# Optimization experiments

Measured on AMD Instinct MI355X. Metric: run time of the kernel, lower is better.

## Reference

```python
import jax, jax.numpy as jnp
import numpy as np
import math

B, T, C = 2, 2048, 1024
H = 16
D = C // H  # 64


def setup_inputs() -> dict:
    key = jax.random.key(0)
    k1, k2, k3 = jax.random.split(key, 3)
    x = jax.random.normal(k1, (B, T, C), dtype=jnp.float32)
    W_attn = jax.random.normal(k2, (3 * C, C), dtype=jnp.float32) * (1.0 / math.sqrt(C))
    W_proj = jax.random.normal(k3, (C, C), dtype=jnp.float32) * (1.0 / math.sqrt(C))
    return {"x": x, "W_attn": W_attn, "W_proj": W_proj}


def reference(x, W_attn, W_proj):
    b, t, c = x.shape
    qkv = x @ W_attn.T                       # [B,T,3C]
    q, k, v = jnp.split(qkv, 3, axis=2)
    # [B,H,T,D]
    q = q.reshape(b, t, H, D).transpose(0, 2, 1, 3)
    k = k.reshape(b, t, H, D).transpose(0, 2, 1, 3)
    v = v.reshape(b, t, H, D).transpose(0, 2, 1, 3)
    scale = 1.0 / math.sqrt(D)
    P = jnp.einsum('bhqd,bhkd->bhqk', q, k) * scale   # [B,H,T,T]
    S = jax.nn.sigmoid(P)
    causal = jnp.tril(jnp.ones((t, t), dtype=bool))   # [T,T]
    S_lower = jnp.where(causal, S, 0.0)
    # suffix (reverse) cumulative sum along key axis
    Z = jax.lax.cumsum(S_lower, axis=3, reverse=True)
    P_prime = P - Z
    P_masked = jnp.where(causal, P_prime, -jnp.inf)
    att = jax.nn.softmax(P_masked, axis=-1)
    y = jnp.einsum('bhqk,bhkd->bhqd', att, v)         # [B,H,T,D]
    y = y.transpose(0, 2, 1, 3).reshape(b, t, c)
    return y @ W_proj.T
```

## Files before the change

### kernel.cpp

```cpp
#include <hip/hip_runtime.h>


typedef _Float16 h8 __attribute__((ext_vector_type(8)));
typedef _Float16 h4 __attribute__((ext_vector_type(4)));
typedef float f4 __attribute__((ext_vector_type(4)));

template <int CTRL>
__device__ __forceinline__ float dpp_shr_self(float x) {
  int xi = __builtin_bit_cast(int, x);
  return __builtin_bit_cast(float,
      __builtin_amdgcn_update_dpp(xi, xi, CTRL, 0xF, 0xF, false));
}
__device__ __forceinline__ float scan16_max(float x) {
  x = fmaxf(x, dpp_shr_self<0x111>(x));
  x = fmaxf(x, dpp_shr_self<0x112>(x));
  x = fmaxf(x, dpp_shr_self<0x114>(x));
  x = fmaxf(x, dpp_shr_self<0x118>(x));
  return x;
}
__device__ __forceinline__ float bcast15(float x) {
  return __builtin_bit_cast(float,
      __builtin_amdgcn_ds_swizzle(__builtin_bit_cast(int, x), 0x01F0));
}

__device__ __forceinline__ void gload_lds16(const _Float16* src, _Float16* dst_lds) {
  __builtin_amdgcn_global_load_lds(
      (const __attribute__((address_space(1))) void*)src,
      (__attribute__((address_space(3))) void*)dst_lds, 16, 0, 0);
}

__device__ __forceinline__ void vmcnt0_fence() {
  asm volatile("s_waitcnt vmcnt(0)" ::: "memory");
  __builtin_amdgcn_sched_barrier(0);
}

__global__ __launch_bounds__(256) void convert_all_kernel(const float* __restrict__ x,
                                                          const float* __restrict__ Wa,
                                                          const float* __restrict__ Wp,
                                                          _Float16* __restrict__ xh,
                                                          _Float16* __restrict__ wah,
                                                          _Float16* __restrict__ wph) {
  int i = blockIdx.x * 256 + threadIdx.x;
  const float* src;
  _Float16* dst;
  int off;
  if (i < 1048576) { src = x; dst = xh; off = i; }
  else if (i < 1048576 + 786432) { src = Wa; dst = wah; off = i - 1048576; }
  else { src = Wp; dst = wph; off = i - (1048576 + 786432); }
  f4 v = *(const f4*)(src + (size_t)off * 4);
  h4 o;
  for (int j = 0; j < 4; ++j) o[j] = (_Float16)v[j];
  *(h4*)(dst + (size_t)off * 4) = o;
}

__global__ __launch_bounds__(512, 2) void gemm1_pipe_kernel(const _Float16* __restrict__ A,
                                                            const _Float16* __restrict__ B,
                                                            _Float16* __restrict__ C,
                                                            int M, int N, int K) {
  __shared__ _Float16 As[2][256 * 64];
  __shared__ _Float16 Bs[2][192 * 64];
  const int tid = threadIdx.x;
  const int wave = tid >> 6, lane = tid & 63;
  const int wm = wave >> 2, wn = wave & 3;
  const int l16 = lane & 15, q4 = lane >> 4;
  const int lrow = lane >> 3, lsc = lane & 7;

  const int xcd = blockIdx.x & 7;
  const int idx = blockIdx.x >> 3;
  const int n_blk = xcd * 2 + (idx & 1);
  const int m_blk = idx >> 1;
  const int m0 = m_blk * 256, n0 = n_blk * 192;

  f4 acc[8][3] = {};

  const int NT = K >> 6;
  {
    const int k0 = 0;
#pragma unroll
    for (int j = 0; j < 4; ++j) {
      const int row = j * 64 + wave * 8 + lrow;
      gload_lds16(A + (size_t)(m0 + row) * K + k0 + (lsc ^ (row & 7)) * 8,
                  &As[0][(j * 64 + wave * 8) * 64]);
    }
#pragma unroll
    for (int j = 0; j < 3; ++j) {
      const int row = j * 64 + wave * 8 + lrow;
      gload_lds16(B + (size_t)(n0 + row) * K + k0 + (lsc ^ (row & 7)) * 8,
                  &Bs[0][(j * 64 + wave * 8) * 64]);
    }
  }
  vmcnt0_fence();
  __builtin_amdgcn_s_barrier();

  int cur = 0;
  for (int kt = 0; kt < NT; ++kt) {
    h8 bf[3][2];
#pragma unroll
    for (int ni = 0; ni < 3; ++ni)
#pragma unroll
      for (int ks = 0; ks < 2; ++ks) {
        const int row = wn * 48 + ni * 16 + l16;
        bf[ni][ks] = *(const h8*)(&Bs[cur][row * 64 + ((ks * 4 + q4) ^ (row & 7)) * 8]);
      }
    if (kt + 1 < NT) {
      const int k0 = (kt + 1) * 64;
      const int nxt = cur ^ 1;
#pragma unroll
      for (int j = 0; j < 4; ++j) {
        const int row = j * 64 + wave * 8 + lrow;
        gload_lds16(A + (size_t)(m0 + row) * K + k0 + (lsc ^ (row & 7)) * 8,
                    &As[nxt][(j * 64 + wave * 8) * 64]);
      }
#pragma unroll
      for (int j = 0; j < 3; ++j) {
        const int row = j * 64 + wave * 8 + lrow;
        gload_lds16(B + (size_t)(n0 + row) * K + k0 + (lsc ^ (row & 7)) * 8,
                    &Bs[nxt][(j * 64 + wave * 8) * 64]);
      }
    }
#pragma unroll
    for (int P = 0; P < 4; ++P) {
      h8 af[2][2];
#pragma unroll
      for (int i = 0; i < 2; ++i)
#pragma unroll
        for (int ks = 0; ks < 2; ++ks) {
          const int row = wm * 128 + (P * 2 + i) * 16 + l16;
          af[i][ks] = *(const h8*)(&As[cur][row * 64 + ((ks * 4 + q4) ^ (row & 7)) * 8]);
        }
      __builtin_amdgcn_s_barrier();
      __builtin_amdgcn_s_setprio(1);
#pragma unroll
      for (int ks = 0; ks < 2; ++ks)
#pragma unroll
        for (int i = 0; i < 2; ++i)
#pragma unroll
          for (int ni = 0; ni < 3; ++ni)
            acc[P * 2 + i][ni] = __builtin_amdgcn_mfma_f32_16x16x32_f16(
                af[i][ks], bf[ni][ks], acc[P * 2 + i][ni], 0, 0, 0);
      __builtin_amdgcn_s_setprio(0);
      if (P == 3 && kt + 1 < NT) vmcnt0_fence();
      __builtin_amdgcn_s_barrier();
    }
    cur ^= 1;
  }
#pragma unroll
  for (int mi = 0; mi < 8; ++mi)
#pragma unroll
    for (int ni = 0; ni < 3; ++ni)
#pragma unroll
      for (int i = 0; i < 4; ++i) {
        int m = m0 + wm * 128 + mi * 16 + q4 * 4 + i;
        int n = n0 + wn * 48 + ni * 16 + l16;
        C[(size_t)m * N + n] = (_Float16)acc[mi][ni][i];
      }
}

template <int BM, int BN, int STRIPE, typename OutT>
__global__ __launch_bounds__(256) void gemm_nt_kernel(const _Float16* __restrict__ A,
                                                      const _Float16* __restrict__ B,
                                                      OutT* __restrict__ C,
                                                      int M, int N, int K) {
  constexpr int MI = BM / 32;
  constexpr int NI = BN / 32;
  __shared__ _Float16 As[BM * 64];
  __shared__ _Float16 Bs[BN * 64];
  const int tid = threadIdx.x;
  const int wave = tid >> 6, lane = tid & 63;
  const int wm = wave >> 1, wn = wave & 1;
  const int l16 = lane & 15, q4 = lane >> 4;
  const int lrow = lane >> 3, lsc = lane & 7;

  const int xcd = blockIdx.x & 7;
  const int idx = blockIdx.x >> 3;
  const int n_blk = xcd * STRIPE + idx % STRIPE;
  const int m_blk = idx / STRIPE;
  const int m0 = m_blk * BM, n0 = n_blk * BN;

  f4 acc[MI][NI] = {};

  for (int k0 = 0; k0 < K; k0 += 64) {
    __syncthreads();
#pragma unroll
    for (int j = 0; j < MI; ++j) {
      const int row = j * 32 + wave * 8 + lrow;
      gload_lds16(A + (size_t)(m0 + row) * K + k0 + (lsc ^ (row & 7)) * 8,
                  As + j * 2048 + wave * 512);
    }
#pragma unroll
    for (int j = 0; j < NI; ++j) {
      const int row = j * 32 + wave * 8 + lrow;
      gload_lds16(B + (size_t)(n0 + row) * K + k0 + (lsc ^ (row & 7)) * 8,
                  Bs + j * 2048 + wave * 512);
    }
    __syncthreads();
#pragma unroll
    for (int ks = 0; ks < 2; ++ks) {
      h8 af[MI], bf[NI];
#pragma unroll
      for (int mi = 0; mi < MI; ++mi) {
        const int row = wm * (BM / 2) + mi * 16 + l16;
        af[mi] = *(const h8*)(As + row * 64 + ((ks * 4 + q4) ^ (row & 7)) * 8);
      }
#pragma unroll
      for (int ni = 0; ni < NI; ++ni) {
        const int row = wn * (BN / 2) + ni * 16 + l16;
        bf[ni] = *(const h8*)(Bs + row * 64 + ((ks * 4 + q4) ^ (row & 7)) * 8);
      }
#pragma unroll
      for (int mi = 0; mi < MI; ++mi)
#pragma unroll
        for (int ni = 0; ni < NI; ++ni)
          acc[mi][ni] = __builtin_amdgcn_mfma_f32_16x16x32_f16(af[mi], bf[ni], acc[mi][ni], 0, 0, 0);
    }
  }
#pragma unroll
  for (int mi = 0; mi < MI; ++mi)
#pragma unroll
    for (int ni = 0; ni < NI; ++ni)
#pragma unroll
      for (int i = 0; i < 4; ++i) {
        int m = m0 + wm * (BM / 2) + mi * 16 + q4 * 4 + i;
        int n = n0 + wn * (BN / 2) + ni * 16 + l16;
        C[(size_t)m * N + n] = (OutT)acc[mi][ni][i];
      }
}

__global__ __launch_bounds__(256, 4) void attn_kernel(const _Float16* __restrict__ qkv,
                                                      _Float16* __restrict__ yh) {
  __shared__ _Float16 Qs[64 * 72];
  __shared__ _Float16 Ks[64 * 72];
  __shared__ _Float16 Vt[64 * 72];
  __shared__ _Float16 Ss[64 * 72];

  const int tid = threadIdx.x;
  const int wave = tid >> 6, lane = tid & 63;
  const int l16 = lane & 15, q = lane >> 4;
  const int qt = 31 - (blockIdx.x >> 5);
  const int bh = blockIdx.x & 31;
  const int b = bh >> 4, h = bh & 15;
  const size_t base = (size_t)b * 2048 * 3072 + h * 64;
  const int rl = 16 * wave + 4 * q;
  const int kt0 = (qt >= 1) ? (qt - 1) : 0;

  h8 Ua, Ub, ONES;
#pragma unroll
  for (int j = 0; j < 8; ++j) {
    int kp = q * 8 + j;
    Ua[j]   = (kp < l16)      ? (_Float16)1.f : (_Float16)0.f;
    Ub[j]   = (kp < 16 + l16) ? (_Float16)1.f : (_Float16)0.f;
    ONES[j] = (_Float16)1.f;
  }

  const int srow0 = tid >> 3, sc8 = tid & 7;
  const int srow1 = srow0 + 32;
  {
    const _Float16 qscale = (_Float16)0.18033688f;
    h8 q0 = *(const h8*)(qkv + base + (size_t)(qt * 64 + srow0) * 3072 + sc8 * 8);
    h8 q1 = *(const h8*)(qkv + base + (size_t)(qt * 64 + srow1) * 3072 + sc8 * 8);
    for (int e = 0; e < 8; ++e) { q0[e] = q0[e] * qscale; q1[e] = q1[e] * qscale; }
    *(h8*)(Qs + srow0 * 72 + sc8 * 8) = q0;
    *(h8*)(Qs + srow1 * 72 + sc8 * 8) = q1;
  }

  h8 kr0, kr1, vr0, vr1;
  {
    const _Float16* kg = qkv + base + (size_t)kt0 * 64 * 3072 + 1024;
    kr0 = *(const h8*)(kg + (size_t)srow0 * 3072 + sc8 * 8);
    kr1 = *(const h8*)(kg + (size_t)srow1 * 3072 + sc8 * 8);
    const _Float16* vg = qkv + base + (size_t)kt0 * 64 * 3072 + 2048 + lane;
    for (int j = 0; j < 8; ++j) vr0[j] = vg[(size_t)(wave * 16 + j) * 3072];
    for (int j = 0; j < 8; ++j) vr1[j] = vg[(size_t)(wave * 16 + 8 + j) * 3072];
  }

  f4 Oacc[4] = {};
  float m_r[4], l_r[4], c_r[4];
#pragma unroll
  for (int i = 0; i < 4; ++i) { m_r[i] = -1e30f; l_r[i] = 0.f; c_r[i] = 0.f; }

  for (int kt = kt0; kt <= qt; ++kt) {
    __syncthreads();
    *(h8*)(Ks + srow0 * 72 + sc8 * 8) = kr0;
    *(h8*)(Ks + srow1 * 72 + sc8 * 8) = kr1;
    *(h8*)(Vt + lane * 72 + wave * 16) = vr0;
    *(h8*)(Vt + lane * 72 + wave * 16 + 8) = vr1;
    __syncthreads();

    if (kt < qt) {
      const _Float16* kg = qkv + base + (size_t)(kt + 1) * 64 * 3072 + 1024;
      kr0 = *(const h8*)(kg + (size_t)srow0 * 3072 + sc8 * 8);
      kr1 = *(const h8*)(kg + (size_t)srow1 * 3072 + sc8 * 8);
      const _Float16* vg = qkv + base + (size_t)(kt + 1) * 64 * 3072 + 2048 + lane;
      for (int j = 0; j < 8; ++j) vr0[j] = vg[(size_t)(wave * 16 + j) * 3072];
      for (int j = 0; j < 8; ++j) vr1[j] = vg[(size_t)(wave * 16 + 8 + j) * 3072];
    }
    const bool diag = (kt == qt);

    f4 pacc[4] = {};
#pragma unroll
    for (int ks = 0; ks < 2; ++ks) {
      h8 af = *(const h8*)(Qs + (16 * wave + l16) * 72 + ks * 32 + q * 8);
#pragma unroll
      for (int ni = 0; ni < 4; ++ni) {
        h8 bf = *(const h8*)(Ks + (16 * ni + l16) * 72 + ks * 32 + q * 8);
        pacc[ni] = __builtin_amdgcn_mfma_f32_16x16x32_f16(af, bf, pacc[ni], 0, 0, 0);
      }
    }

#pragma unroll
    for (int ni = 0; ni < 4; ++ni) {
      const int col = 16 * ni + l16;
#pragma unroll
      for (int i = 0; i < 4; ++i) {
        float e = __builtin_amdgcn_exp2f(-pacc[ni][i]);
        float s = __builtin_amdgcn_rcpf(1.f + e) * 1.44269504f;
        if (diag && col > rl + i) s = 0.f;
        Ss[(rl + i) * 72 + col] = (_Float16)s;
      }
    }
    f4 ex[4], tot;
    {
      h8 s0 = *(const h8*)(Ss + (16 * wave + l16) * 72 + q * 8);
      h8 s1 = *(const h8*)(Ss + (16 * wave + l16) * 72 + 32 + q * 8);
      f4 z = {};
      f4 t0 = __builtin_amdgcn_mfma_f32_16x16x32_f16(s0, ONES, z, 0, 0, 0);
      ex[0] = __builtin_amdgcn_mfma_f32_16x16x32_f16(s0, Ua, z, 0, 0, 0);
      ex[1] = __builtin_amdgcn_mfma_f32_16x16x32_f16(s0, Ub, z, 0, 0, 0);
      ex[2] = __builtin_amdgcn_mfma_f32_16x16x32_f16(s1, Ua, t0, 0, 0, 0);
      ex[3] = __builtin_amdgcn_mfma_f32_16x16x32_f16(s1, Ub, t0, 0, 0, 0);
      tot   = __builtin_amdgcn_mfma_f32_16x16x32_f16(s1, ONES, t0, 0, 0, 0);
    }
    float rmax[4];
#pragma unroll
    for (int i = 0; i < 4; ++i) {
      float L0 = pacc[0][i] + (c_r[i] + ex[0][i]);
      float L1 = pacc[1][i] + (c_r[i] + ex[1][i]);
      float L2 = pacc[2][i] + (c_r[i] + ex[2][i]);
      float L3 = pacc[3][i] + (c_r[i] + ex[3][i]);
      if (diag) {
        if (0  + l16 > rl + i) L0 = -1e30f;
        if (16 + l16 > rl + i) L1 = -1e30f;
        if (32 + l16 > rl + i) L2 = -1e30f;
        if (48 + l16 > rl + i) L3 = -1e30f;
      }
      pacc[0][i] = L0; pacc[1][i] = L1; pacc[2][i] = L2; pacc[3][i] = L3;
      rmax[i] = fmaxf(fmaxf(L0, L1), fmaxf(L2, L3));
      c_r[i] += tot[i];
    }
    float mn[4], al[4];
#pragma unroll
    for (int i = 0; i < 4; ++i) {
      float gm = bcast15(scan16_max(rmax[i]));
      mn[i] = fmaxf(m_r[i], gm);
      al[i] = __builtin_amdgcn_exp2f(m_r[i] - mn[i]);
      m_r[i] = mn[i];
    }
#pragma unroll
    for (int ni = 0; ni < 4; ++ni)
#pragma unroll
      for (int i = 0; i < 4; ++i) {
        float w = __builtin_amdgcn_exp2f(pacc[ni][i] - mn[i]);
        Ss[(rl + i) * 72 + 16 * ni + l16] = (_Float16)w;
      }
#pragma unroll
    for (int ni = 0; ni < 4; ++ni)
#pragma unroll
      for (int i = 0; i < 4; ++i) Oacc[ni][i] *= al[i];
    {
      h8 w0 = *(const h8*)(Ss + (16 * wave + l16) * 72 + q * 8);
      h8 w1 = *(const h8*)(Ss + (16 * wave + l16) * 72 + 32 + q * 8);
      f4 z = {};
      f4 la = __builtin_amdgcn_mfma_f32_16x16x32_f16(w0, ONES, z, 0, 0, 0);
      la = __builtin_amdgcn_mfma_f32_16x16x32_f16(w1, ONES, la, 0, 0, 0);
#pragma unroll
      for (int i = 0; i < 4; ++i) l_r[i] = l_r[i] * al[i] + la[i];
#pragma unroll
      for (int ni = 0; ni < 4; ++ni) {
        h8 bf0 = *(const h8*)(Vt + (16 * ni + l16) * 72 + q * 8);
        Oacc[ni] = __builtin_amdgcn_mfma_f32_16x16x32_f16(w0, bf0, Oacc[ni], 0, 0, 0);
        h8 bf1 = *(const h8*)(Vt + (16 * ni + l16) * 72 + 32 + q * 8);
        Oacc[ni] = __builtin_amdgcn_mfma_f32_16x16x32_f16(w1, bf1, Oacc[ni], 0, 0, 0);
      }
    }
  }

#pragma unroll
  for (int ni = 0; ni < 4; ++ni)
#pragma unroll
    for (int i = 0; i < 4; ++i) {
      int t = qt * 64 + rl + i;
      float yv = Oacc[ni][i] * __builtin_amdgcn_rcpf(l_r[i]);
      yh[((size_t)(b * 2048 + t)) * 1024 + h * 64 + 16 * ni + l16] = (_Float16)yv;
    }
}

extern "C" void kernel_launch(void* const* d_in, const int* in_sizes, int n_in,
                              void* d_out, int out_size, void* d_ws, size_t ws_size,
                              hipStream_t stream) {
  const float* x  = (const float*)d_in[0];
  const float* Wa = (const float*)d_in[1];
  const float* Wp = (const float*)d_in[2];
  float* out = (float*)d_out;

  char* ws = (char*)d_ws;
  _Float16* xh   = (_Float16*)(ws);
  _Float16* wah  = (_Float16*)(ws + 8388608);
  _Float16* wph  = (_Float16*)(ws + 14680064);
  _Float16* qkvh = (_Float16*)(ws + 16777216);
  _Float16* yh   = (_Float16*)(ws + 41943040);

  convert_all_kernel<<<8192, 256, 0, stream>>>(x, Wa, Wp, xh, wah, wph);

  gemm1_pipe_kernel<<<256, 512, 0, stream>>>(xh, wah, qkvh, 4096, 3072, 1024);

  attn_kernel<<<1024, 256, 0, stream>>>(qkvh, yh);

  gemm_nt_kernel<64, 128, 1, float>
      <<<512, 256, 0, stream>>>(yh, wph, out, 4096, 1024, 1024);
}
```

Measured before the change: 148.5 us.

## Interleave QKV GEMM tile loads across sub-phases with partial vmcnt waits

Spreads the global-to-LDS loads of the next K tile across the four MFMA sub-phases instead of issuing them all at once. Full vmcnt(0) waits become partial waits (vmcnt 2/4), and the per-phase barriers shrink to one mid-iteration barrier plus one at the end. The goal is to overlap memory traffic with MFMA work and cut barrier stalls. Correctness now depends on the load order matching the rows each phase reads, and the mid-iteration wait ties the A rows of phases 2-3 to load completion.

```diff
diff --git a/kernel.cpp b/kernel.cpp
--- a/kernel.cpp
+++ b/kernel.cpp
@@ -29,9 +29,20 @@
       (__attribute__((address_space(3))) void*)dst_lds, 16, 0, 0);
 }
 
-__device__ __forceinline__ void vmcnt0_fence() {
+__device__ __forceinline__ void vm_wait0() {
   asm volatile("s_waitcnt vmcnt(0)" ::: "memory");
   __builtin_amdgcn_sched_barrier(0);
+}
+__device__ __forceinline__ void vm_wait2() {
+  asm volatile("s_waitcnt vmcnt(2)" ::: "memory");
+  __builtin_amdgcn_sched_barrier(0);
+}
+__device__ __forceinline__ void vm_wait4() {
+  asm volatile("s_waitcnt vmcnt(4)" ::: "memory");
+  __builtin_amdgcn_sched_barrier(0);
+}
+__device__ __forceinline__ void vmem_order_fence() {
+  __builtin_amdgcn_sched_barrier(0x38F);
 }
 
 __global__ __launch_bounds__(256) void convert_all_kernel(const float* __restrict__ x,
@@ -74,26 +85,30 @@
   f4 acc[8][3] = {};
 
   const int NT = K >> 6;
-  {
-    const int k0 = 0;
-#pragma unroll
-    for (int j = 0; j < 4; ++j) {
-      const int row = j * 64 + wave * 8 + lrow;
-      gload_lds16(A + (size_t)(m0 + row) * K + k0 + (lsc ^ (row & 7)) * 8,
-                  &As[0][(j * 64 + wave * 8) * 64]);
-    }
-#pragma unroll
-    for (int j = 0; j < 3; ++j) {
-      const int row = j * 64 + wave * 8 + lrow;
-      gload_lds16(B + (size_t)(n0 + row) * K + k0 + (lsc ^ (row & 7)) * 8,
-                  &Bs[0][(j * 64 + wave * 8) * 64]);
-    }
-  }
-  vmcnt0_fence();
+
+  auto stageA = [&](int buf, int j, int k0) {
+    const int row = j * 64 + wave * 8 + lrow;
+    gload_lds16(A + (size_t)(m0 + row) * K + k0 + (lsc ^ (row & 7)) * 8,
+                &As[buf][(j * 64 + wave * 8) * 64]);
+  };
+  auto stageB = [&](int buf, int j, int k0) {
+    const int row = j * 64 + wave * 8 + lrow;
+    gload_lds16(B + (size_t)(n0 + row) * K + k0 + (lsc ^ (row & 7)) * 8,
+                &Bs[buf][(j * 64 + wave * 8) * 64]);
+  };
+
+  stageB(0, 0, 0); stageB(0, 1, 0); stageB(0, 2, 0); stageA(0, 0, 0); stageA(0, 2, 0);
+  vmem_order_fence();
+  stageA(0, 1, 0); stageA(0, 3, 0);
+  vm_wait2();
   __builtin_amdgcn_s_barrier();
 
   int cur = 0;
   for (int kt = 0; kt < NT; ++kt) {
+    const bool more = (kt + 1 < NT);
+    const int nxt = cur ^ 1;
+    const int k1 = (kt + 1) << 6;
+
     h8 bf[3][2];
 #pragma unroll
     for (int ni = 0; ni < 3; ++ni)
@@ -102,24 +117,20 @@
         const int row = wn * 48 + ni * 16 + l16;
         bf[ni][ks] = *(const h8*)(&Bs[cur][row * 64 + ((ks * 4 + q4) ^ (row & 7)) * 8]);
       }
-    if (kt + 1 < NT) {
-      const int k0 = (kt + 1) * 64;
-      const int nxt = cur ^ 1;
-#pragma unroll
-      for (int j = 0; j < 4; ++j) {
-        const int row = j * 64 + wave * 8 + lrow;
-        gload_lds16(A + (size_t)(m0 + row) * K + k0 + (lsc ^ (row & 7)) * 8,
-                    &As[nxt][(j * 64 + wave * 8) * 64]);
-      }
-#pragma unroll
-      for (int j = 0; j < 3; ++j) {
-        const int row = j * 64 + wave * 8 + lrow;
-        gload_lds16(B + (size_t)(n0 + row) * K + k0 + (lsc ^ (row & 7)) * 8,
-                    &Bs[nxt][(j * 64 + wave * 8) * 64]);
-      }
-    }
+
 #pragma unroll
     for (int P = 0; P < 4; ++P) {
+      if (more) {
+        if (P == 0) { stageB(nxt, 0, k1); stageB(nxt, 1, k1); }
+        if (P == 1) { stageB(nxt, 2, k1); stageA(nxt, 0, k1); }
+        if (P == 2) { stageA(nxt, 2, k1); }
+        if (P == 3) { stageA(nxt, 1, k1); stageA(nxt, 3, k1); }
+        vmem_order_fence();
+      }
+      if (P == 2) {
+        if (more) vm_wait4(); else vm_wait0();
+        __builtin_amdgcn_s_barrier();
+      }
       h8 af[2][2];
 #pragma unroll
       for (int i = 0; i < 2; ++i)
@@ -128,7 +139,6 @@
           const int row = wm * 128 + (P * 2 + i) * 16 + l16;
           af[i][ks] = *(const h8*)(&As[cur][row * 64 + ((ks * 4 + q4) ^ (row & 7)) * 8]);
         }
-      __builtin_amdgcn_s_barrier();
       __builtin_amdgcn_s_setprio(1);
 #pragma unroll
       for (int ks = 0; ks < 2; ++ks)
@@ -139,9 +149,9 @@
             acc[P * 2 + i][ni] = __builtin_amdgcn_mfma_f32_16x16x32_f16(
                 af[i][ks], bf[ni][ks], acc[P * 2 + i][ni], 0, 0, 0);
       __builtin_amdgcn_s_setprio(0);
-      if (P == 3 && kt + 1 < NT) vmcnt0_fence();
-      __builtin_amdgcn_s_barrier();
-    }
+    }
+    if (more) vm_wait2();
+    __builtin_amdgcn_s_barrier();
     cur ^= 1;
   }
 #pragma unroll
```

After: 153.2 us. 1.03x slower.
